# Optimization experiments

Measured on AMD Instinct MI355X. Metric: run time of the kernel, lower is better.

## Reference

```python
import jax, jax.numpy as jnp
import numpy as np

B, H = 1, 512
NVAR, NCLS = 16384, 65536
NP, NM = 4096, 4096
NEG = -1e30


def setup_inputs() -> dict:
    key = jax.random.key(0)
    ks = jax.random.split(key, 16)
    s = 0.02  # weight init scale
    return {
        "literal_emb": jax.random.normal(ks[0], (B, 2 * NVAR, H), jnp.float32),
        "clause_emb": jax.random.normal(ks[1], (B, NCLS, H), jnp.float32),
        "pos_idx": jax.random.randint(ks[2], (NP,), 0, NCLS),
        "neg_idx": jax.random.randint(ks[3], (NM,), 0, NCLS),
        "keep_mask": jax.random.randint(ks[4], (NP, NM), 0, 2).astype(bool),
        "taken_mask": jax.random.uniform(ks[5], (NP, NM)) < 0.01,  # sparse exclusion set
        "var_K_w": s * jax.random.normal(ks[6], (H, H), jnp.float32),
        "var_K_b": jnp.zeros((H,), jnp.float32),
        "var_Q_w": s * jax.random.normal(ks[7], (H, H), jnp.float32),
        "var_Q_b": jnp.zeros((H,), jnp.float32),
        "var_attn_w": s * jax.random.normal(ks[8], (1, H), jnp.float32),
        "var_attn_b": jnp.zeros((1,), jnp.float32),
        "W_Q_w": s * jax.random.normal(ks[9], (H, H), jnp.float32),
        "W_Q_b": jnp.zeros((H,), jnp.float32),
        "W_K_w": s * jax.random.normal(ks[10], (H, H), jnp.float32),
        "W_K_b": jnp.zeros((H,), jnp.float32),
    }


def reference(literal_emb, clause_emb, pos_idx, neg_idx, keep_mask, taken_mask,
              var_K_w, var_K_b, var_Q_w, var_Q_b, var_attn_w, var_attn_b,
              W_Q_w, W_Q_b, W_K_w, W_K_b):
    n_vars = literal_emb.shape[1] // 2
    # --- select_var: additive attention over positive literals ---
    K = literal_emb[:, :n_vars]                       # [B, V, H]
    K_t = K @ var_K_w.T + var_K_b                     # [B, V, H]
    Q = clause_emb.sum(axis=1)                        # [B, H] (C_aggr='sum')
    Q_t = Q @ var_Q_w.T + var_Q_b                     # [B, H]
    u = (jnp.tanh(K_t + Q_t[:, None, :]) @ var_attn_w.T + var_attn_b)[..., 0]  # [B, V]
    log_score = jax.nn.log_softmax(u, axis=-1)
    var_logp = jnp.max(log_score, axis=-1)            # [B]
    var_idx = jnp.argmax(log_score, axis=-1)          # [B]
    # --- clause-pair attention over pivot pos/neg clause pools ---
    q = clause_emb[:, pos_idx] @ W_Q_w.T + W_Q_b      # [B, NP, H]
    k = clause_emb[:, neg_idx] @ W_K_w.T + W_K_b      # [B, NM, H]
    h = q.shape[-1]
    scores = jnp.einsum('bnh,bmh->bnm', q, k) / jnp.sqrt(jnp.float32(h))
    # mask_grid_asym: drop invalid (keep_mask==0) and already-taken pairs, log-normalize
    valid = keep_mask & (~taken_mask)                 # [NP, NM]
    masked = jnp.where(valid[None], scores, jnp.float32(NEG))
    flat = masked.reshape(masked.shape[0], -1)        # [B, NP*NM]
    logp = jax.nn.log_softmax(flat, axis=-1)
    C_logp = jnp.max(logp, axis=-1)                   # [B]
    C_flat = jnp.argmax(logp, axis=-1)                # [B]
    M = scores.shape[-1]
    ci, cj = C_flat // M, C_flat % M
    c_idx_pos = pos_idx[ci]                           # map back to global clause ids
    c_idx_neg = neg_idx[cj]
    c_logp = C_logp + var_logp                        # [B]
    return (c_logp, c_idx_pos, c_idx_neg, var_idx)
```

## Files before the change

kernel.cpp:

```cpp
#include <hip/hip_runtime.h>
#include <hip/hip_bf16.h>
#include <math.h>

#define HH 512
#define NVARS 16384
#define NPOS 4096
#define NMS 4096
#define NEGV -1.0e30f
#define RSQRT_H 0.04419417382415922f

typedef unsigned short u16;
typedef unsigned char u8;
typedef __attribute__((ext_vector_type(8))) short bf16x8;
typedef __attribute__((ext_vector_type(4))) float f32x4;

struct SPart { float m; float s; int a; int pad; };

__device__ inline u16 f2bf(float f) {
  unsigned u = __float_as_uint(f);
  unsigned r = (u + 0x7fffu + ((u >> 16) & 1u)) >> 16;
  return (u16)r;
}
__device__ inline float bf2f(u16 h) { return __uint_as_float(((unsigned)h) << 16); }

__device__ inline void wreduce_maxidx(float& v, int& idx) {
#pragma unroll
  for (int m = 1; m < 64; m <<= 1) {
    float ov = __shfl_xor(v, m, 64);
    int oi = __shfl_xor(idx, m, 64);
    if (ov > v || (ov == v && oi < idx)) { v = ov; idx = oi; }
  }
}

__device__ inline float wreduce_sum(float v) {
#pragma unroll
  for (int m = 1; m < 64; m <<= 1) v += __shfl_xor(v, m, 64);
  return v;
}

__device__ __forceinline__ void stage_frag(const u16* src, u16* dst) {
  __builtin_amdgcn_global_load_lds(
      (const __attribute__((address_space(1))) void*)src,
      (__attribute__((address_space(3))) void*)dst, 16, 0, 0);
}

__device__ __forceinline__ void do_tofrag(
    const float* __restrict__ src, u16* __restrict__ hi, u16* __restrict__ lo,
    int frag, int lane) {
  const int R = frag >> 4, K = frag & 15;
  const float* p = src + (size_t)(R * 16 + (lane & 15)) * HH + K * 32 + (lane >> 4) * 8;
  float v[8];
  *(float4*)&v[0] = *(const float4*)p;
  *(float4*)&v[4] = *(const float4*)(p + 4);
  u16 h[8], l[8];
#pragma unroll
  for (int e = 0; e < 8; ++e) { h[e] = f2bf(v[e]); l[e] = f2bf(v[e] - bf2f(h[e])); }
  size_t base = (size_t)frag * 512 + (size_t)lane * 8;
  *(ushort4*)(hi + base) = *(ushort4*)&h[0];
  *(ushort4*)(hi + base + 4) = *(ushort4*)&h[4];
  *(ushort4*)(lo + base) = *(ushort4*)&l[0];
  *(ushort4*)(lo + base + 4) = *(ushort4*)&l[4];
}

#define MFMA16(A, B)                                                                 \
  _Pragma("unroll") for (int i_ = 0; i_ < 4; ++i_)                                   \
  _Pragma("unroll") for (int j_ = 0; j_ < 4; ++j_)                                   \
    acc[i_][j_] = __builtin_amdgcn_mfma_f32_16x16x32_bf16(A[i_], B[j_], acc[i_][j_], 0, 0, 0);

#define MFMAS(AH, AL, BH, BL)                                                        \
  do { MFMA16(AH, BH) MFMA16(AH, BL) MFMA16(AL, BH) } while (0)

#define LOADF(s, AH, AL, BH, BL, PAH, PAL, PBH, PBL)                                 \
  do {                                                                               \
    _Pragma("unroll") for (int f_ = 0; f_ < 4; ++f_) {                               \
      size_t oa_ = abase + (size_t)f_ * 8192 + (size_t)(s) * 512;                    \
      size_t ob_ = bbase + (size_t)f_ * 8192 + (size_t)(s) * 512;                    \
      AH[f_] = *(const bf16x8*)(PAH + oa_);                                          \
      AL[f_] = *(const bf16x8*)(PAL + oa_);                                          \
      BH[f_] = *(const bf16x8*)(PBH + ob_);                                          \
      BL[f_] = *(const bf16x8*)(PBL + ob_);                                          \
    }                                                                                \
  } while (0)

__global__ __launch_bounds__(256) void wtofrag_kernel(
    const float* __restrict__ varKw, u16* __restrict__ wkhi, u16* __restrict__ wklo,
    const float* __restrict__ WQw, u16* __restrict__ pwqhi, u16* __restrict__ pwqlo,
    const float* __restrict__ WKw, u16* __restrict__ pwkhi, u16* __restrict__ pwklo) {
  const int wb = blockIdx.x;
  const int m = wb >> 7;
  const int frag = (wb & 127) * 4 + (threadIdx.x >> 6);
  const float* src = (m == 0) ? varKw : (m == 1) ? WQw : WKw;
  u16* hi = (m == 0) ? wkhi : (m == 1) ? pwqhi : pwkhi;
  u16* lo = (m == 0) ? wklo : (m == 1) ? pwqlo : pwklo;
  do_tofrag(src, hi, lo, frag, threadIdx.x & 63);
}

__global__ __launch_bounds__(256, 3) void proj_kernel(
    const float* __restrict__ clause,
    const int* __restrict__ pos_idx, const int* __restrict__ neg_idx,
    const u16* __restrict__ pwqhi, const u16* __restrict__ pwqlo,
    const u16* __restrict__ pwkhi, const u16* __restrict__ pwklo,
    const float* __restrict__ bQ, const float* __restrict__ bK,
    u16* __restrict__ qhi, u16* __restrict__ qlo,
    u16* __restrict__ khi, u16* __restrict__ klo) {
  const int* __restrict__ idx = blockIdx.z ? neg_idx : pos_idx;
  const u16* __restrict__ whp = blockIdx.z ? pwkhi : pwqhi;
  const u16* __restrict__ wlp = blockIdx.z ? pwklo : pwqlo;
  const float* __restrict__ bias = blockIdx.z ? bK : bQ;
  u16* __restrict__ ohi = blockIdx.z ? khi : qhi;
  u16* __restrict__ olo = blockIdx.z ? klo : qlo;

  const int t = threadIdx.x, lane = t & 63, wid = t >> 6;
  const int wn = wid & 1, wm = wid >> 1;
  const int row0 = blockIdx.x * 128;
  const int col0 = blockIdx.y * 128;

  const float* bptr[4];
#pragma unroll
  for (int j = 0; j < 4; ++j) {
    int g = idx[row0 + wn * 64 + j * 16 + (lane & 15)];
    bptr[j] = clause + (size_t)g * HH + (lane >> 4) * 8;
  }
  const size_t abase = (size_t)((col0 >> 4) + wm * 4) * 8192 + (size_t)lane * 8;

  f32x4 acc[4][4] = {};
#pragma unroll
  for (int s = 0; s < 16; ++s) {
    float rB[4][8];
    bf16x8 aH[4], aL[4], bH[4], bL[4];
#pragma unroll
    for (int f = 0; f < 4; ++f) {
      *(float4*)&rB[f][0] = *(const float4*)(bptr[f] + s * 32);
      *(float4*)&rB[f][4] = *(const float4*)(bptr[f] + s * 32 + 4);
      size_t oa = abase + (size_t)f * 8192 + (size_t)s * 512;
      aH[f] = *(const bf16x8*)(whp + oa);
      aL[f] = *(const bf16x8*)(wlp + oa);
    }
#pragma unroll
    for (int f = 0; f < 4; ++f)
#pragma unroll
      for (int e = 0; e < 8; ++e) {
        float v = rB[f][e];
        u16 h = f2bf(v);
        bH[f][e] = (short)h;
        bL[f][e] = (short)f2bf(v - bf2f(h));
      }
    MFMA16(aH, bH)
    MFMA16(aL, bH)
    MFMA16(aH, bL)
  }

  const int q4 = lane >> 4;
#pragma unroll
  for (int i = 0; i < 4; ++i) {
    const int hbase = col0 + wm * 64 + i * 16 + q4 * 4;
    float b0 = bias[hbase + 0], b1 = bias[hbase + 1];
    float b2 = bias[hbase + 2], b3 = bias[hbase + 3];
    const int lane16 = (lane & 15) + ((i & 1) * 2 + (q4 >> 1)) * 16;
    const int sub = (q4 & 1) * 4;
#pragma unroll
    for (int j = 0; j < 4; ++j) {
      const int frag = ((row0 + wn * 64 + j * 16) >> 4) * 16 +
                       ((col0 + wm * 64 + i * 16) >> 5);
      size_t base = (size_t)frag * 512 + (size_t)lane16 * 8 + sub;
      ushort4 hv, lv;
      float v;
      v = acc[i][j][0] + b0; hv.x = f2bf(v); lv.x = f2bf(v - bf2f(hv.x));
      v = acc[i][j][1] + b1; hv.y = f2bf(v); lv.y = f2bf(v - bf2f(hv.y));
      v = acc[i][j][2] + b2; hv.z = f2bf(v); lv.z = f2bf(v - bf2f(hv.z));
      v = acc[i][j][3] + b3; hv.w = f2bf(v); lv.w = f2bf(v - bf2f(hv.w));
      *(ushort4*)(ohi + base) = hv;
      *(ushort4*)(olo + base) = lv;
    }
  }
}

__global__ __launch_bounds__(256, 3) void mega_kernel(
    const u16* __restrict__ qhi, const u16* __restrict__ qlo,
    const u16* __restrict__ khi, const u16* __restrict__ klo,
    const void* __restrict__ keep, const void* __restrict__ taken,
    SPart* __restrict__ parts,
    const float* __restrict__ clause, double* __restrict__ qpart,
    const float* __restrict__ lit, u16* __restrict__ lithi, u16* __restrict__ litlo) {
  __shared__ unsigned long long mrow[128][2];
  __shared__ float s_rv[4]; __shared__ int s_ri[4]; __shared__ float s_rs[4];
  __shared__ float s_bm; __shared__ int s_ba;

  const int id = blockIdx.x;
  const int t = threadIdx.x;
  const int lane = t & 63;
  const int wid = t >> 6;

  if (id >= 3072) {
    const int frag = (id - 3072) * 4 + wid;
    do_tofrag(lit, lithi, litlo, frag, lane);
    return;
  }
  if (id >= 1024) {
    const int qb = id - 1024;
    const int fg = t & 127;
    const int rh = t >> 7;
    const float* base = clause + ((size_t)qb * 32 + rh * 16) * HH + fg * 4;
    float4 v[16];
#pragma unroll
    for (int u = 0; u < 16; ++u)
      v[u] = *(const float4*)(base + (size_t)u * HH);
    double a0 = 0.0, a1 = 0.0, a2 = 0.0, a3 = 0.0;
#pragma unroll
    for (int u = 0; u < 16; ++u) {
      a0 += (double)v[u].x; a1 += (double)v[u].y;
      a2 += (double)v[u].z; a3 += (double)v[u].w;
    }
    double* o = qpart + (size_t)(qb * 2 + rh) * HH + fg * 4;
    o[0] = a0; o[1] = a1; o[2] = a2; o[3] = a3;
    return;
  }

  const int wn = wid & 1, wm = wid >> 1;

  const int bid = id;
  const int xcd = bid & 7, p = bid >> 3;
  const int sp = p >> 6, q = p & 63;
  const int g = xcd * 2 + sp;
  const int bx = (g & 3) * 8 + (q & 7);
  const int by = (g >> 2) * 8 + (q >> 3);

  const int n0 = by * 128;
  const int m0 = bx * 128;

  {
    const int r = t >> 1, half = t & 1;
    const unsigned* kw = (const unsigned*)keep;
    int f = 1;
#pragma unroll
    for (int i = 0; i < 16; ++i) f &= (kw[i] <= 1u);
    unsigned long long w = 0;
    if (!f) {
      const u8* kp = (const u8*)keep + (size_t)(n0 + r) * NMS + m0 + half * 64;
      const u8* tp = (const u8*)taken + (size_t)(n0 + r) * NMS + m0 + half * 64;
#pragma unroll
      for (int c = 0; c < 4; ++c) {
        uint4 kv = *(const uint4*)(kp + c * 16);
        uint4 tv = *(const uint4*)(tp + c * 16);
        unsigned kws[4] = {kv.x, kv.y, kv.z, kv.w};
        unsigned tws[4] = {tv.x, tv.y, tv.z, tv.w};
#pragma unroll
        for (int wi = 0; wi < 4; ++wi)
#pragma unroll
          for (int y = 0; y < 4; ++y) {
            unsigned kb = (kws[wi] >> (8 * y)) & 0xffu;
            unsigned tb = (tws[wi] >> (8 * y)) & 0xffu;
            w |= (unsigned long long)(kb && !tb) << (c * 16 + wi * 4 + y);
          }
      }
    } else {
      const unsigned* kp = (const unsigned*)keep + (size_t)(n0 + r) * NMS + m0 + half * 64;
      const unsigned* tp = (const unsigned*)taken + (size_t)(n0 + r) * NMS + m0 + half * 64;
#pragma unroll
      for (int c = 0; c < 16; ++c) {
        uint4 kv = *(const uint4*)(kp + c * 4);
        uint4 tv = *(const uint4*)(tp + c * 4);
        w |= (unsigned long long)(kv.x && !tv.x) << (c * 4 + 0);
        w |= (unsigned long long)(kv.y && !tv.y) << (c * 4 + 1);
        w |= (unsigned long long)(kv.z && !tv.z) << (c * 4 + 2);
        w |= (unsigned long long)(kv.w && !tv.w) << (c * 4 + 3);
      }
    }
    mrow[r][half] = w;
  }

  const size_t abase = (size_t)((n0 >> 4) + wn * 4) * 8192 + (size_t)lane * 8;
  const size_t bbase = (size_t)((m0 >> 4) + wm * 4) * 8192 + (size_t)lane * 8;

  f32x4 acc[4][4] = {};
#pragma unroll
  for (int s = 0; s < 16; ++s) {
    bf16x8 aH[4], aL[4], bH[4], bL[4];
    LOADF(s, aH, aL, bH, bL, qhi, qlo, khi, klo);
    MFMAS(aH, aL, bH, bL);
  }
  __syncthreads();

  const int rbase = wn * 64 + (lane >> 4) * 4;
  const int cb15 = (lane & 15);

  float mv = NEGV; int mi = 0x7fffffff;
#pragma unroll
  for (int i = 0; i < 4; ++i) {
#pragma unroll
    for (int r = 0; r < 4; ++r) {
      int rl = rbase + i * 16 + r;
      unsigned long long ww = mrow[rl][wm];
      int gb = (n0 + rl) * NMS + m0;
#pragma unroll
      for (int j = 0; j < 4; ++j) {
        int bit = j * 16 + cb15;
        int cl = wm * 64 + bit;
        float sv = acc[i][j][r] * RSQRT_H;
        acc[i][j][r] = sv;
        bool valid = ((ww >> bit) & 1ull) != 0;
        if (valid && (sv > mv || (sv == mv && gb + cl < mi))) { mv = sv; mi = gb + cl; }
      }
    }
  }
  wreduce_maxidx(mv, mi);
  if ((t & 63) == 0) { s_rv[wid] = mv; s_ri[wid] = mi; }
  __syncthreads();
  if (t == 0) {
    float bm = s_rv[0]; int ba = s_ri[0];
    for (int w = 1; w < 4; ++w)
      if (s_rv[w] > bm || (s_rv[w] == bm && s_ri[w] < ba)) { bm = s_rv[w]; ba = s_ri[w]; }
    s_bm = bm; s_ba = ba;
  }
  __syncthreads();
  const float bm = s_bm;

  float se = 0.f;
#pragma unroll
  for (int i = 0; i < 4; ++i) {
#pragma unroll
    for (int r = 0; r < 4; ++r) {
      int rl = rbase + i * 16 + r;
      unsigned long long ww = mrow[rl][wm];
#pragma unroll
      for (int j = 0; j < 4; ++j) {
        int bit = j * 16 + cb15;
        bool valid = ((ww >> bit) & 1ull) != 0;
        if (valid) se += __expf(acc[i][j][r] - bm);
      }
    }
  }
  se = wreduce_sum(se);
  if ((t & 63) == 0) s_rs[wid] = se;
  __syncthreads();
  if (t == 0) {
    SPart pt;
    pt.m = s_bm;
    pt.s = s_rs[0] + s_rs[1] + s_rs[2] + s_rs[3];
    pt.a = s_ba; pt.pad = 0;
    parts[by * 32 + bx] = pt;
  }
}

__global__ __launch_bounds__(256) void qred_kernel(
    const double* __restrict__ qpart, double* __restrict__ Qd) {
  __shared__ double red[256];
  const int t = threadIdx.x;
  const int h = blockIdx.x * 16 + (t & 15);
  const int chunk = t >> 4;
  double s = 0.0;
  for (int j0 = 0; j0 < 256; j0 += 8) {
    double v[8];
#pragma unroll
    for (int u = 0; u < 8; ++u)
      v[u] = qpart[(size_t)(chunk * 256 + j0 + u) * HH + h];
#pragma unroll
    for (int u = 0; u < 8; ++u) s += v[u];
  }
  red[t] = s;
  __syncthreads();
  for (int off = 8; off > 0; off >>= 1) {
    if (chunk < off) red[t] += red[t + off * 16];
    __syncthreads();
  }
  if (t < 16) Qd[blockIdx.x * 16 + t] = red[t];
}

__global__ __launch_bounds__(256) void prepmv_kernel(
    const double* __restrict__ Qd, const float* __restrict__ varQw,
    const float* __restrict__ varQb, const float* __restrict__ varKb,
    float* __restrict__ tvec) {
  __shared__ double red[256];
  const int t = threadIdx.x;
  const int h = blockIdx.x * 16 + (t & 15);
  const int chunk = t >> 4;
  const float* wrow = varQw + (size_t)h * HH + chunk * 32;
  const double* qd = Qd + chunk * 32;
  double s = 0.0;
  for (int j = 0; j < 32; ++j) s += qd[j] * (double)wrow[j];
  red[t] = s;
  __syncthreads();
  for (int off = 8; off > 0; off >>= 1) {
    if (chunk < off) red[t] += red[t + off * 16];
    __syncthreads();
  }
  if (t < 16) {
    int hh = blockIdx.x * 16 + t;
    tvec[hh] = (float)(red[t] + (double)varQb[hh] + (double)varKb[hh]);
  }
}

__global__ __launch_bounds__(256, 2) void ktu_kernel(
    const u16* __restrict__ lithi, const u16* __restrict__ litlo,
    const u16* __restrict__ wkhi, const u16* __restrict__ wklo,
    const float* __restrict__ tvec, const float* __restrict__ attnw,
    float* __restrict__ upart) {
  __shared__ __align__(16) u16 lds[2][4][8][512];
  const int t = threadIdx.x, lane = t & 63, wid = t >> 6;
  const int wn = wid & 1, wm = wid >> 1;
  const int row0 = blockIdx.x * 128;
  const int l8 = lane * 8;

  const u16* sa = (wid == 0) ? lithi : (wid == 1) ? litlo : (wid == 2) ? wkhi : wklo;
  const int rb = (wid < 2) ? (row0 >> 4) : (blockIdx.y * 8);
  const u16* sab = sa + (size_t)rb * 8192 + l8;

#define KSTAGE(buf, s)                                                        \
  _Pragma("unroll") for (int f_ = 0; f_ < 8; ++f_)                            \
    stage_frag(sab + (size_t)f_ * 8192 + (size_t)(s) * 512,                   \
               &lds[buf][wid][f_][0]);

  KSTAGE(0, 0)
  f32x4 acc[4][4] = {};
#pragma unroll
  for (int s = 0; s < 16; ++s) {
    __syncthreads();
    if (s < 15) { KSTAGE((s + 1) & 1, s + 1) }
    const int b = s & 1;
    bf16x8 aH[4], aL[4], bH[4], bL[4];
#pragma unroll
    for (int f = 0; f < 4; ++f) {
      aH[f] = *(const bf16x8*)&lds[b][0][wn * 4 + f][l8];
      aL[f] = *(const bf16x8*)&lds[b][1][wn * 4 + f][l8];
      bH[f] = *(const bf16x8*)&lds[b][2][wm * 4 + f][l8];
      bL[f] = *(const bf16x8*)&lds[b][3][wm * 4 + f][l8];
    }
    MFMAS(aH, aL, bH, bL);
  }
#undef KSTAGE

  const int cbase = blockIdx.y * 128 + wm * 64;
  float tv[4], aw[4];
#pragma unroll
  for (int j = 0; j < 4; ++j) {
    int c = cbase + j * 16 + (lane & 15);
    tv[j] = tvec[c]; aw[j] = attnw[c];
  }
  float us[4][4];
#pragma unroll
  for (int i = 0; i < 4; ++i)
#pragma unroll
    for (int r = 0; r < 4; ++r) {
      float s = 0.f;
#pragma unroll
      for (int j = 0; j < 4; ++j) {
        float x = acc[i][j][r] + tv[j];
        float th = 1.0f - 2.0f / (__expf(2.0f * x) + 1.0f);
        s += th * aw[j];
      }
      us[i][r] = s;
    }
#pragma unroll
  for (int m = 1; m < 16; m <<= 1)
#pragma unroll
    for (int i = 0; i < 4; ++i)
#pragma unroll
      for (int r = 0; r < 4; ++r) us[i][r] += __shfl_xor(us[i][r], m, 64);
  if ((lane & 15) == 0) {
#pragma unroll
    for (int i = 0; i < 4; ++i)
#pragma unroll
      for (int r = 0; r < 4; ++r) {
        int row = row0 + wn * 64 + i * 16 + (lane >> 4) * 4 + r;
        upart[(size_t)(blockIdx.y * 2 + wm) * NVARS + row] = us[i][r];
      }
  }
}

__global__ __launch_bounds__(256) void usum_kernel(
    const float* __restrict__ upart, SPart* __restrict__ uparts2) {
  __shared__ float s_rv[4]; __shared__ int s_ri[4]; __shared__ float s_rs[4];
  __shared__ float s_bm; __shared__ int s_ba;
  const int t = threadIdx.x;
  const int i = blockIdx.x * 256 + t;
  float u = 0.f;
#pragma unroll
  for (int p = 0; p < 8; ++p) u += upart[(size_t)p * NVARS + i];
  float mv = u; int mi = i;
  wreduce_maxidx(mv, mi);
  if ((t & 63) == 0) { s_rv[t >> 6] = mv; s_ri[t >> 6] = mi; }
  __syncthreads();
  if (t == 0) {
    float bm = s_rv[0]; int ba = s_ri[0];
    for (int w = 1; w < 4; ++w)
      if (s_rv[w] > bm || (s_rv[w] == bm && s_ri[w] < ba)) { bm = s_rv[w]; ba = s_ri[w]; }
    s_bm = bm; s_ba = ba;
  }
  __syncthreads();
  float se = __expf(u - s_bm);
  se = wreduce_sum(se);
  if ((t & 63) == 0) s_rs[t >> 6] = se;
  __syncthreads();
  if (t == 0) {
    SPart p;
    p.m = s_bm;
    p.s = s_rs[0] + s_rs[1] + s_rs[2] + s_rs[3];
    p.a = s_ba; p.pad = 0;
    uparts2[blockIdx.x] = p;
  }
}

__global__ __launch_bounds__(256) void final_kernel(
    const SPart* __restrict__ uparts2, const SPart* __restrict__ parts,
    const int* __restrict__ pos_idx, const int* __restrict__ neg_idx,
    float* __restrict__ out) {
  __shared__ float s_rv[4]; __shared__ int s_ri[4]; __shared__ float s_rs[4];
  __shared__ float s_umax; __shared__ int s_uarg; __shared__ float s_usum;
  __shared__ float s_gm; __shared__ int s_ga;
  const int t = threadIdx.x;

  float mv = -3.0e38f; int mi = 0x7fffffff;
  SPart up;
  if (t < 64) {
    up = uparts2[t];
    mv = up.m; mi = up.a;
  }
  wreduce_maxidx(mv, mi);
  if ((t & 63) == 0) { s_rv[t >> 6] = mv; s_ri[t >> 6] = mi; }
  __syncthreads();
  if (t == 0) {
    float bm = s_rv[0]; int ba = s_ri[0];
    for (int w = 1; w < 4; ++w)
      if (s_rv[w] > bm || (s_rv[w] == bm && s_ri[w] < ba)) { bm = s_rv[w]; ba = s_ri[w]; }
    s_umax = bm; s_uarg = ba;
  }
  __syncthreads();
  float se = (t < 64) ? up.s * __expf(up.m - s_umax) : 0.f;
  se = wreduce_sum(se);
  if ((t & 63) == 0) s_rs[t >> 6] = se;
  __syncthreads();
  if (t == 0) s_usum = s_rs[0] + s_rs[1] + s_rs[2] + s_rs[3];
  __syncthreads();

  mv = NEGV; mi = 0x7fffffff;
  for (int i = t; i < 1024; i += 256) {
    SPart p = parts[i];
    if (p.m > mv || (p.m == mv && p.a < mi)) { mv = p.m; mi = p.a; }
  }
  wreduce_maxidx(mv, mi);
  if ((t & 63) == 0) { s_rv[t >> 6] = mv; s_ri[t >> 6] = mi; }
  __syncthreads();
  if (t == 0) {
    float bm = s_rv[0]; int ba = s_ri[0];
    for (int w = 1; w < 4; ++w)
      if (s_rv[w] > bm || (s_rv[w] == bm && s_ri[w] < ba)) { bm = s_rv[w]; ba = s_ri[w]; }
    s_gm = bm; s_ga = ba;
  }
  __syncthreads();
  const float gm = s_gm;
  float ss = 0.f;
  for (int i = t; i < 1024; i += 256) {
    SPart p = parts[i];
    ss += p.s * __expf(p.m - gm);
  }
  ss = wreduce_sum(ss);
  if ((t & 63) == 0) s_rs[t >> 6] = ss;
  __syncthreads();
  if (t == 0) {
    float gsum = s_rs[0] + s_rs[1] + s_rs[2] + s_rs[3];
    float c_logp = -logf(gsum) - logf(s_usum);
    int ga = s_ga;
    if (ga == 0x7fffffff) ga = 0;
    int ci = ga >> 12, cj = ga & 4095;
    out[0] = c_logp;
    out[1] = (float)pos_idx[ci];
    out[2] = (float)neg_idx[cj];
    out[3] = (float)s_uarg;
  }
}

extern "C" void kernel_launch(void* const* d_in, const int* in_sizes, int n_in,
                              void* d_out, int out_size, void* d_ws, size_t ws_size,
                              hipStream_t stream) {
  (void)in_sizes; (void)n_in; (void)out_size; (void)ws_size;
  const float* lit    = (const float*)d_in[0];
  const float* clause = (const float*)d_in[1];
  const int* pos_idx  = (const int*)d_in[2];
  const int* neg_idx  = (const int*)d_in[3];
  const void* keep    = d_in[4];
  const void* taken   = d_in[5];
  const float* varKw  = (const float*)d_in[6];
  const float* varKb  = (const float*)d_in[7];
  const float* varQw  = (const float*)d_in[8];
  const float* varQb  = (const float*)d_in[9];
  const float* attnw  = (const float*)d_in[10];
  const float* WQw    = (const float*)d_in[12];
  const float* WQb    = (const float*)d_in[13];
  const float* WKw    = (const float*)d_in[14];
  const float* WKb    = (const float*)d_in[15];

  char* ws = (char*)d_ws;
  size_t off = 0;
  auto alloc = [&](size_t b) {
    char* p = ws + off;
    off = (off + b + 255) & ~(size_t)255;
    return p;
  };
  double* qpart              = (double*)alloc((size_t)4096 * HH * 8);
  double* Qd                 = (double*)alloc(HH * 8);
  float* tvec                = (float*)alloc(HH * 4);
  float* upart               = (float*)alloc(8 * (size_t)NVARS * 4);
  u16* qhi                   = (u16*)alloc((size_t)NPOS * HH * 2);
  u16* qlo                   = (u16*)alloc((size_t)NPOS * HH * 2);
  u16* khi                   = (u16*)alloc((size_t)NMS * HH * 2);
  u16* klo                   = (u16*)alloc((size_t)NMS * HH * 2);
  u16* wkhi                  = (u16*)alloc((size_t)HH * HH * 2);
  u16* wklo                  = (u16*)alloc((size_t)HH * HH * 2);
  u16* pwqhi                 = (u16*)alloc((size_t)HH * HH * 2);
  u16* pwqlo                 = (u16*)alloc((size_t)HH * HH * 2);
  u16* pwkhi                 = (u16*)alloc((size_t)HH * HH * 2);
  u16* pwklo                 = (u16*)alloc((size_t)HH * HH * 2);
  u16* lithi                 = (u16*)alloc((size_t)NVARS * HH * 2);
  u16* litlo                 = (u16*)alloc((size_t)NVARS * HH * 2);
  SPart* parts               = (SPart*)alloc(1024 * sizeof(SPart));
  SPart* uparts2             = (SPart*)alloc(64 * sizeof(SPart));

  wtofrag_kernel<<<384, 256, 0, stream>>>(varKw, wkhi, wklo,
                                          WQw, pwqhi, pwqlo,
                                          WKw, pwkhi, pwklo);
  proj_kernel<<<dim3(32, 4, 2), 256, 0, stream>>>(clause, pos_idx, neg_idx,
                                                  pwqhi, pwqlo, pwkhi, pwklo,
                                                  WQb, WKb,
                                                  qhi, qlo, khi, klo);
  mega_kernel<<<7168, 256, 0, stream>>>(qhi, qlo, khi, klo, keep, taken, parts,
                                        clause, qpart, lit, lithi, litlo);
  qred_kernel<<<32, 256, 0, stream>>>(qpart, Qd);
  prepmv_kernel<<<32, 256, 0, stream>>>(Qd, varQw, varQb, varKb, tvec);
  ktu_kernel<<<dim3(128, 4), 256, 0, stream>>>(lithi, litlo, wkhi, wklo,
                                               tvec, attnw, upart);
  usum_kernel<<<64, 256, 0, stream>>>(upart, uparts2);
  final_kernel<<<1, 256, 0, stream>>>(uparts2, parts, pos_idx, neg_idx,
                                      (float*)d_out);
}
```

Baseline: 258.2 us.

## Regroup kernels: fuse projection with prep work, scores with var attention

The q/k projection now runs in the same launch as the clause-sum and literal-to-fragment conversion (megaA). The clause-pair score GEMM with masked max/sum-exp now shares a launch with the literal key GEMM and tanh attention (megaB). The score GEMM also switches from direct global fragment loads to LDS double-buffered staging. This cuts launches and lets independent work fill the GPU together, at the cost of more LDS per block in megaB, which may lower occupancy.

Result: faster. 214.0 us (-17.1%).

```diff
diff --git a/kernel.cpp b/kernel.cpp
--- a/kernel.cpp
+++ b/kernel.cpp
@@ -69,18 +69,6 @@
 
 #define MFMAS(AH, AL, BH, BL)                                                        \
   do { MFMA16(AH, BH) MFMA16(AH, BL) MFMA16(AL, BH) } while (0)
-
-#define LOADF(s, AH, AL, BH, BL, PAH, PAL, PBH, PBL)                                 \
-  do {                                                                               \
-    _Pragma("unroll") for (int f_ = 0; f_ < 4; ++f_) {                               \
-      size_t oa_ = abase + (size_t)f_ * 8192 + (size_t)(s) * 512;                    \
-      size_t ob_ = bbase + (size_t)f_ * 8192 + (size_t)(s) * 512;                    \
-      AH[f_] = *(const bf16x8*)(PAH + oa_);                                          \
-      AL[f_] = *(const bf16x8*)(PAL + oa_);                                          \
-      BH[f_] = *(const bf16x8*)(PBH + ob_);                                          \
-      BL[f_] = *(const bf16x8*)(PBL + ob_);                                          \
-    }                                                                                \
-  } while (0)
 
 __global__ __launch_bounds__(256) void wtofrag_kernel(
     const float* __restrict__ varKw, u16* __restrict__ wkhi, u16* __restrict__ wklo,
@@ -95,25 +83,57 @@
   do_tofrag(src, hi, lo, frag, threadIdx.x & 63);
 }
 
-__global__ __launch_bounds__(256, 3) void proj_kernel(
+__global__ __launch_bounds__(256, 3) void megaA_kernel(
     const float* __restrict__ clause,
     const int* __restrict__ pos_idx, const int* __restrict__ neg_idx,
     const u16* __restrict__ pwqhi, const u16* __restrict__ pwqlo,
     const u16* __restrict__ pwkhi, const u16* __restrict__ pwklo,
     const float* __restrict__ bQ, const float* __restrict__ bK,
     u16* __restrict__ qhi, u16* __restrict__ qlo,
-    u16* __restrict__ khi, u16* __restrict__ klo) {
-  const int* __restrict__ idx = blockIdx.z ? neg_idx : pos_idx;
-  const u16* __restrict__ whp = blockIdx.z ? pwkhi : pwqhi;
-  const u16* __restrict__ wlp = blockIdx.z ? pwklo : pwqlo;
-  const float* __restrict__ bias = blockIdx.z ? bK : bQ;
-  u16* __restrict__ ohi = blockIdx.z ? khi : qhi;
-  u16* __restrict__ olo = blockIdx.z ? klo : qlo;
-
-  const int t = threadIdx.x, lane = t & 63, wid = t >> 6;
+    u16* __restrict__ khi, u16* __restrict__ klo,
+    double* __restrict__ qpart,
+    const float* __restrict__ lit, u16* __restrict__ lithi, u16* __restrict__ litlo) {
+  const int id = blockIdx.x;
+  const int t = threadIdx.x;
+  const int lane = t & 63, wid = t >> 6;
+
+  if (id >= 2304) {
+    const int frag = (id - 2304) * 4 + wid;
+    do_tofrag(lit, lithi, litlo, frag, lane);
+    return;
+  }
+  if (id >= 256) {
+    const int qb = id - 256;
+    const int fg = t & 127;
+    const int rh = t >> 7;
+    const float* base = clause + ((size_t)qb * 32 + rh * 16) * HH + fg * 4;
+    float4 v[16];
+#pragma unroll
+    for (int u = 0; u < 16; ++u)
+      v[u] = *(const float4*)(base + (size_t)u * HH);
+    double a0 = 0.0, a1 = 0.0, a2 = 0.0, a3 = 0.0;
+#pragma unroll
+    for (int u = 0; u < 16; ++u) {
+      a0 += (double)v[u].x; a1 += (double)v[u].y;
+      a2 += (double)v[u].z; a3 += (double)v[u].w;
+    }
+    double* o = qpart + (size_t)(qb * 2 + rh) * HH + fg * 4;
+    o[0] = a0; o[1] = a1; o[2] = a2; o[3] = a3;
+    return;
+  }
+
+  const int pid = id;
+  const int rowt = pid & 31, colt = (pid >> 5) & 3, z = pid >> 7;
+  const int* __restrict__ idx = z ? neg_idx : pos_idx;
+  const u16* __restrict__ whp = z ? pwkhi : pwqhi;
+  const u16* __restrict__ wlp = z ? pwklo : pwqlo;
+  const float* __restrict__ bias = z ? bK : bQ;
+  u16* __restrict__ ohi = z ? khi : qhi;
+  u16* __restrict__ olo = z ? klo : qlo;
+
   const int wn = wid & 1, wm = wid >> 1;
-  const int row0 = blockIdx.x * 128;
-  const int col0 = blockIdx.y * 128;
+  const int row0 = rowt * 128;
+  const int col0 = colt * 128;
 
   const float* bptr[4];
 #pragma unroll
@@ -172,173 +192,6 @@
       *(ushort4*)(ohi + base) = hv;
       *(ushort4*)(olo + base) = lv;
     }
-  }
-}
-
-__global__ __launch_bounds__(256, 3) void mega_kernel(
-    const u16* __restrict__ qhi, const u16* __restrict__ qlo,
-    const u16* __restrict__ khi, const u16* __restrict__ klo,
-    const void* __restrict__ keep, const void* __restrict__ taken,
-    SPart* __restrict__ parts,
-    const float* __restrict__ clause, double* __restrict__ qpart,
-    const float* __restrict__ lit, u16* __restrict__ lithi, u16* __restrict__ litlo) {
-  __shared__ unsigned long long mrow[128][2];
-  __shared__ float s_rv[4]; __shared__ int s_ri[4]; __shared__ float s_rs[4];
-  __shared__ float s_bm; __shared__ int s_ba;
-
-  const int id = blockIdx.x;
-  const int t = threadIdx.x;
-  const int lane = t & 63;
-  const int wid = t >> 6;
-
-  if (id >= 3072) {
-    const int frag = (id - 3072) * 4 + wid;
-    do_tofrag(lit, lithi, litlo, frag, lane);
-    return;
-  }
-  if (id >= 1024) {
-    const int qb = id - 1024;
-    const int fg = t & 127;
-    const int rh = t >> 7;
-    const float* base = clause + ((size_t)qb * 32 + rh * 16) * HH + fg * 4;
-    float4 v[16];
-#pragma unroll
-    for (int u = 0; u < 16; ++u)
-      v[u] = *(const float4*)(base + (size_t)u * HH);
-    double a0 = 0.0, a1 = 0.0, a2 = 0.0, a3 = 0.0;
-#pragma unroll
-    for (int u = 0; u < 16; ++u) {
-      a0 += (double)v[u].x; a1 += (double)v[u].y;
-      a2 += (double)v[u].z; a3 += (double)v[u].w;
-    }
-    double* o = qpart + (size_t)(qb * 2 + rh) * HH + fg * 4;
-    o[0] = a0; o[1] = a1; o[2] = a2; o[3] = a3;
-    return;
-  }
-
-  const int wn = wid & 1, wm = wid >> 1;
-
-  const int bid = id;
-  const int xcd = bid & 7, p = bid >> 3;
-  const int sp = p >> 6, q = p & 63;
-  const int g = xcd * 2 + sp;
-  const int bx = (g & 3) * 8 + (q & 7);
-  const int by = (g >> 2) * 8 + (q >> 3);
-
-  const int n0 = by * 128;
-  const int m0 = bx * 128;
-
-  {
-    const int r = t >> 1, half = t & 1;
-    const unsigned* kw = (const unsigned*)keep;
-    int f = 1;
-#pragma unroll
-    for (int i = 0; i < 16; ++i) f &= (kw[i] <= 1u);
-    unsigned long long w = 0;
-    if (!f) {
-      const u8* kp = (const u8*)keep + (size_t)(n0 + r) * NMS + m0 + half * 64;
-      const u8* tp = (const u8*)taken + (size_t)(n0 + r) * NMS + m0 + half * 64;
-#pragma unroll
-      for (int c = 0; c < 4; ++c) {
-        uint4 kv = *(const uint4*)(kp + c * 16);
-        uint4 tv = *(const uint4*)(tp + c * 16);
-        unsigned kws[4] = {kv.x, kv.y, kv.z, kv.w};
-        unsigned tws[4] = {tv.x, tv.y, tv.z, tv.w};
-#pragma unroll
-        for (int wi = 0; wi < 4; ++wi)
-#pragma unroll
-          for (int y = 0; y < 4; ++y) {
-            unsigned kb = (kws[wi] >> (8 * y)) & 0xffu;
-            unsigned tb = (tws[wi] >> (8 * y)) & 0xffu;
-            w |= (unsigned long long)(kb && !tb) << (c * 16 + wi * 4 + y);
-          }
-      }
-    } else {
-      const unsigned* kp = (const unsigned*)keep + (size_t)(n0 + r) * NMS + m0 + half * 64;
-      const unsigned* tp = (const unsigned*)taken + (size_t)(n0 + r) * NMS + m0 + half * 64;
-#pragma unroll
-      for (int c = 0; c < 16; ++c) {
-        uint4 kv = *(const uint4*)(kp + c * 4);
-        uint4 tv = *(const uint4*)(tp + c * 4);
-        w |= (unsigned long long)(kv.x && !tv.x) << (c * 4 + 0);
-        w |= (unsigned long long)(kv.y && !tv.y) << (c * 4 + 1);
-        w |= (unsigned long long)(kv.z && !tv.z) << (c * 4 + 2);
-        w |= (unsigned long long)(kv.w && !tv.w) << (c * 4 + 3);
-      }
-    }
-    mrow[r][half] = w;
-  }
-
-  const size_t abase = (size_t)((n0 >> 4) + wn * 4) * 8192 + (size_t)lane * 8;
-  const size_t bbase = (size_t)((m0 >> 4) + wm * 4) * 8192 + (size_t)lane * 8;
-
-  f32x4 acc[4][4] = {};
-#pragma unroll
-  for (int s = 0; s < 16; ++s) {
-    bf16x8 aH[4], aL[4], bH[4], bL[4];
-    LOADF(s, aH, aL, bH, bL, qhi, qlo, khi, klo);
-    MFMAS(aH, aL, bH, bL);
-  }
-  __syncthreads();
-
-  const int rbase = wn * 64 + (lane >> 4) * 4;
-  const int cb15 = (lane & 15);
-
-  float mv = NEGV; int mi = 0x7fffffff;
-#pragma unroll
-  for (int i = 0; i < 4; ++i) {
-#pragma unroll
-    for (int r = 0; r < 4; ++r) {
-      int rl = rbase + i * 16 + r;
-      unsigned long long ww = mrow[rl][wm];
-      int gb = (n0 + rl) * NMS + m0;
-#pragma unroll
-      for (int j = 0; j < 4; ++j) {
-        int bit = j * 16 + cb15;
-        int cl = wm * 64 + bit;
-        float sv = acc[i][j][r] * RSQRT_H;
-        acc[i][j][r] = sv;
-        bool valid = ((ww >> bit) & 1ull) != 0;
-        if (valid && (sv > mv || (sv == mv && gb + cl < mi))) { mv = sv; mi = gb + cl; }
-      }
-    }
-  }
-  wreduce_maxidx(mv, mi);
-  if ((t & 63) == 0) { s_rv[wid] = mv; s_ri[wid] = mi; }
-  __syncthreads();
-  if (t == 0) {
-    float bm = s_rv[0]; int ba = s_ri[0];
-    for (int w = 1; w < 4; ++w)
-      if (s_rv[w] > bm || (s_rv[w] == bm && s_ri[w] < ba)) { bm = s_rv[w]; ba = s_ri[w]; }
-    s_bm = bm; s_ba = ba;
-  }
-  __syncthreads();
-  const float bm = s_bm;
-
-  float se = 0.f;
-#pragma unroll
-  for (int i = 0; i < 4; ++i) {
-#pragma unroll
-    for (int r = 0; r < 4; ++r) {
-      int rl = rbase + i * 16 + r;
-      unsigned long long ww = mrow[rl][wm];
-#pragma unroll
-      for (int j = 0; j < 4; ++j) {
-        int bit = j * 16 + cb15;
-        bool valid = ((ww >> bit) & 1ull) != 0;
-        if (valid) se += __expf(acc[i][j][r] - bm);
-      }
-    }
-  }
-  se = wreduce_sum(se);
-  if ((t & 63) == 0) s_rs[wid] = se;
-  __syncthreads();
-  if (t == 0) {
-    SPart pt;
-    pt.m = s_bm;
-    pt.s = s_rs[0] + s_rs[1] + s_rs[2] + s_rs[3];
-    pt.a = s_ba; pt.pad = 0;
-    parts[by * 32 + bx] = pt;
   }
 }
 
@@ -390,32 +243,165 @@
   }
 }
 
-__global__ __launch_bounds__(256, 2) void ktu_kernel(
+__global__ __launch_bounds__(256, 2) void megaB_kernel(
+    const u16* __restrict__ qhi, const u16* __restrict__ qlo,
+    const u16* __restrict__ khi, const u16* __restrict__ klo,
+    const void* __restrict__ keep, const void* __restrict__ taken,
+    SPart* __restrict__ parts,
     const u16* __restrict__ lithi, const u16* __restrict__ litlo,
     const u16* __restrict__ wkhi, const u16* __restrict__ wklo,
     const float* __restrict__ tvec, const float* __restrict__ attnw,
     float* __restrict__ upart) {
   __shared__ __align__(16) u16 lds[2][4][8][512];
-  const int t = threadIdx.x, lane = t & 63, wid = t >> 6;
+  __shared__ unsigned long long mrow[128][2];
+  __shared__ float s_rv[4]; __shared__ int s_ri[4]; __shared__ float s_rs[4];
+  __shared__ float s_bm; __shared__ int s_ba;
+
+  const int id = blockIdx.x;
+  const int t = threadIdx.x;
+  const int lane = t & 63;
+  const int wid = t >> 6;
   const int wn = wid & 1, wm = wid >> 1;
-  const int row0 = blockIdx.x * 128;
   const int l8 = lane * 8;
 
-  const u16* sa = (wid == 0) ? lithi : (wid == 1) ? litlo : (wid == 2) ? wkhi : wklo;
-  const int rb = (wid < 2) ? (row0 >> 4) : (blockIdx.y * 8);
+  if (id >= 1024) {
+    const int kb = id - 1024;
+    const int rowt = kb >> 2, ht = kb & 3;
+    const int row0 = rowt * 128;
+
+    const u16* sa = (wid == 0) ? lithi : (wid == 1) ? litlo : (wid == 2) ? wkhi : wklo;
+    const int rb = (wid < 2) ? (row0 >> 4) : (ht * 8);
+    const u16* sab = sa + (size_t)rb * 8192 + l8;
+
+#define KSTAGE(buf, s)                                                        \
+    _Pragma("unroll") for (int f_ = 0; f_ < 8; ++f_)                          \
+      stage_frag(sab + (size_t)f_ * 8192 + (size_t)(s) * 512,                 \
+                 &lds[buf][wid][f_][0]);
+
+    KSTAGE(0, 0)
+    f32x4 acc[4][4] = {};
+#pragma unroll
+    for (int s = 0; s < 16; ++s) {
+      __syncthreads();
+      if (s < 15) { KSTAGE((s + 1) & 1, s + 1) }
+      const int b = s & 1;
+      bf16x8 aH[4], aL[4], bH[4], bL[4];
+#pragma unroll
+      for (int f = 0; f < 4; ++f) {
+        aH[f] = *(const bf16x8*)&lds[b][0][wn * 4 + f][l8];
+        aL[f] = *(const bf16x8*)&lds[b][1][wn * 4 + f][l8];
+        bH[f] = *(const bf16x8*)&lds[b][2][wm * 4 + f][l8];
+        bL[f] = *(const bf16x8*)&lds[b][3][wm * 4 + f][l8];
+      }
+      MFMAS(aH, aL, bH, bL);
+    }
+#undef KSTAGE
+
+    const int cbase = ht * 128 + wm * 64;
+    float tv[4], aw[4];
+#pragma unroll
+    for (int j = 0; j < 4; ++j) {
+      int c = cbase + j * 16 + (lane & 15);
+      tv[j] = tvec[c]; aw[j] = attnw[c];
+    }
+    float us[4][4];
+#pragma unroll
+    for (int i = 0; i < 4; ++i)
+#pragma unroll
+      for (int r = 0; r < 4; ++r) {
+        float s = 0.f;
+#pragma unroll
+        for (int j = 0; j < 4; ++j) {
+          float x = acc[i][j][r] + tv[j];
+          float th = 1.0f - 2.0f / (__expf(2.0f * x) + 1.0f);
+          s += th * aw[j];
+        }
+        us[i][r] = s;
+      }
+#pragma unroll
+    for (int m = 1; m < 16; m <<= 1)
+#pragma unroll
+      for (int i = 0; i < 4; ++i)
+#pragma unroll
+        for (int r = 0; r < 4; ++r) us[i][r] += __shfl_xor(us[i][r], m, 64);
+    if ((lane & 15) == 0) {
+#pragma unroll
+      for (int i = 0; i < 4; ++i)
+#pragma unroll
+        for (int r = 0; r < 4; ++r) {
+          int row = row0 + wn * 64 + i * 16 + (lane >> 4) * 4 + r;
+          upart[(size_t)(ht * 2 + wm) * NVARS + row] = us[i][r];
+        }
+    }
+    return;
+  }
+
+  const int bid = id;
+  const int xcd = bid & 7, p = bid >> 3;
+  const int sp = p >> 6, q = p & 63;
+  const int g = xcd * 2 + sp;
+  const int bx = (g & 3) * 8 + (q & 7);
+  const int by = (g >> 2) * 8 + (q >> 3);
+
+  const int n0 = by * 128;
+  const int m0 = bx * 128;
+
+  {
+    const int r = t >> 1, half = t & 1;
+    const unsigned* kw = (const unsigned*)keep;
+    int f = 1;
+#pragma unroll
+    for (int i = 0; i < 16; ++i) f &= (kw[i] <= 1u);
+    unsigned long long w = 0;
+    if (!f) {
+      const u8* kp = (const u8*)keep + (size_t)(n0 + r) * NMS + m0 + half * 64;
+      const u8* tp = (const u8*)taken + (size_t)(n0 + r) * NMS + m0 + half * 64;
+#pragma unroll
+      for (int c = 0; c < 4; ++c) {
+        uint4 kv = *(const uint4*)(kp + c * 16);
+        uint4 tv = *(const uint4*)(tp + c * 16);
+        unsigned kws[4] = {kv.x, kv.y, kv.z, kv.w};
+        unsigned tws[4] = {tv.x, tv.y, tv.z, tv.w};
+#pragma unroll
+        for (int wi = 0; wi < 4; ++wi)
+#pragma unroll
+          for (int y = 0; y < 4; ++y) {
+            unsigned kb = (kws[wi] >> (8 * y)) & 0xffu;
+            unsigned tb = (tws[wi] >> (8 * y)) & 0xffu;
+            w |= (unsigned long long)(kb && !tb) << (c * 16 + wi * 4 + y);
+          }
+      }
+    } else {
+      const unsigned* kp = (const unsigned*)keep + (size_t)(n0 + r) * NMS + m0 + half * 64;
+      const unsigned* tp = (const unsigned*)taken + (size_t)(n0 + r) * NMS + m0 + half * 64;
+#pragma unroll
+      for (int c = 0; c < 16; ++c) {
+        uint4 kv = *(const uint4*)(kp + c * 4);
+        uint4 tv = *(const uint4*)(tp + c * 4);
+        w |= (unsigned long long)(kv.x && !tv.x) << (c * 4 + 0);
+        w |= (unsigned long long)(kv.y && !tv.y) << (c * 4 + 1);
+        w |= (unsigned long long)(kv.z && !tv.z) << (c * 4 + 2);
+        w |= (unsigned long long)(kv.w && !tv.w) << (c * 4 + 3);
+      }
+    }
+    mrow[r][half] = w;
+  }
+
+  const u16* sa = (wid == 0) ? qhi : (wid == 1) ? qlo : (wid == 2) ? khi : klo;
+  const int rb = (wid < 2) ? (n0 >> 4) : (m0 >> 4);
   const u16* sab = sa + (size_t)rb * 8192 + l8;
 
-#define KSTAGE(buf, s)                                                        \
+#define SSTAGE(buf, s)                                                        \
   _Pragma("unroll") for (int f_ = 0; f_ < 8; ++f_)                            \
     stage_frag(sab + (size_t)f_ * 8192 + (size_t)(s) * 512,                   \
                &lds[buf][wid][f_][0]);
 
-  KSTAGE(0, 0)
+  SSTAGE(0, 0)
   f32x4 acc[4][4] = {};
 #pragma unroll
   for (int s = 0; s < 16; ++s) {
     __syncthreads();
-    if (s < 15) { KSTAGE((s + 1) & 1, s + 1) }
+    if (s < 15) { SSTAGE((s + 1) & 1, s + 1) }
     const int b = s & 1;
     bf16x8 aH[4], aL[4], bH[4], bL[4];
 #pragma unroll
@@ -427,43 +413,66 @@
     }
     MFMAS(aH, aL, bH, bL);
   }
-#undef KSTAGE
-
-  const int cbase = blockIdx.y * 128 + wm * 64;
-  float tv[4], aw[4];
-#pragma unroll
-  for (int j = 0; j < 4; ++j) {
-    int c = cbase + j * 16 + (lane & 15);
-    tv[j] = tvec[c]; aw[j] = attnw[c];
-  }
-  float us[4][4];
-#pragma unroll
-  for (int i = 0; i < 4; ++i)
+#undef SSTAGE
+
+  const int rbase = wn * 64 + (lane >> 4) * 4;
+  const int cb15 = (lane & 15);
+
+  float mv = NEGV; int mi = 0x7fffffff;
+#pragma unroll
+  for (int i = 0; i < 4; ++i) {
 #pragma unroll
     for (int r = 0; r < 4; ++r) {
-      float s = 0.f;
+      int rl = rbase + i * 16 + r;
+      unsigned long long ww = mrow[rl][wm];
+      int gb = (n0 + rl) * NMS + m0;
 #pragma unroll
       for (int j = 0; j < 4; ++j) {
-        float x = acc[i][j][r] + tv[j];
-        float th = 1.0f - 2.0f / (__expf(2.0f * x) + 1.0f);
-        s += th * aw[j];
+        int bit = j * 16 + cb15;
+        int cl = wm * 64 + bit;
+        float sv = acc[i][j][r] * RSQRT_H;
+        acc[i][j][r] = sv;
+        bool valid = ((ww >> bit) & 1ull) != 0;
+        if (valid && (sv > mv || (sv == mv && gb + cl < mi))) { mv = sv; mi = gb + cl; }
       }
-      us[i][r] = s;
-    }
-#pragma unroll
-  for (int m = 1; m < 16; m <<= 1)
-#pragma unroll
-    for (int i = 0; i < 4; ++i)
-#pragma unroll
-      for (int r = 0; r < 4; ++r) us[i][r] += __shfl_xor(us[i][r], m, 64);
-  if ((lane & 15) == 0) {
-#pragma unroll
-    for (int i = 0; i < 4; ++i)
-#pragma unroll
-      for (int r = 0; r < 4; ++r) {
-        int row = row0 + wn * 64 + i * 16 + (lane >> 4) * 4 + r;
-        upart[(size_t)(blockIdx.y * 2 + wm) * NVARS + row] = us[i][r];
+    }
+  }
+  wreduce_maxidx(mv, mi);
+  if ((t & 63) == 0) { s_rv[wid] = mv; s_ri[wid] = mi; }
+  __syncthreads();
+  if (t == 0) {
+    float bm = s_rv[0]; int ba = s_ri[0];
+    for (int w = 1; w < 4; ++w)
+      if (s_rv[w] > bm || (s_rv[w] == bm && s_ri[w] < ba)) { bm = s_rv[w]; ba = s_ri[w]; }
+    s_bm = bm; s_ba = ba;
+  }
+  __syncthreads();
+  const float bm = s_bm;
+
+  float se = 0.f;
+#pragma unroll
+  for (int i = 0; i < 4; ++i) {
+#pragma unroll
+    for (int r = 0; r < 4; ++r) {
+      int rl = rbase + i * 16 + r;
+      unsigned long long ww = mrow[rl][wm];
+#pragma unroll
+      for (int j = 0; j < 4; ++j) {
+        int bit = j * 16 + cb15;
+        bool valid = ((ww >> bit) & 1ull) != 0;
+        if (valid) se += __expf(acc[i][j][r] - bm);
       }
+    }
+  }
+  se = wreduce_sum(se);
+  if ((t & 63) == 0) s_rs[wid] = se;
+  __syncthreads();
+  if (t == 0) {
+    SPart pt;
+    pt.m = s_bm;
+    pt.s = s_rs[0] + s_rs[1] + s_rs[2] + s_rs[3];
+    pt.a = s_ba; pt.pad = 0;
+    parts[by * 32 + bx] = pt;
   }
 }
 
@@ -618,16 +627,15 @@
   wtofrag_kernel<<<384, 256, 0, stream>>>(varKw, wkhi, wklo,
                                           WQw, pwqhi, pwqlo,
                                           WKw, pwkhi, pwklo);
-  proj_kernel<<<dim3(32, 4, 2), 256, 0, stream>>>(clause, pos_idx, neg_idx,
-                                                  pwqhi, pwqlo, pwkhi, pwklo,
-                                                  WQb, WKb,
-                                                  qhi, qlo, khi, klo);
-  mega_kernel<<<7168, 256, 0, stream>>>(qhi, qlo, khi, klo, keep, taken, parts,
-                                        clause, qpart, lit, lithi, litlo);
+  megaA_kernel<<<6400, 256, 0, stream>>>(clause, pos_idx, neg_idx,
+                                         pwqhi, pwqlo, pwkhi, pwklo,
+                                         WQb, WKb, qhi, qlo, khi, klo,
+                                         qpart, lit, lithi, litlo);
   qred_kernel<<<32, 256, 0, stream>>>(qpart, Qd);
   prepmv_kernel<<<32, 256, 0, stream>>>(Qd, varQw, varQb, varKb, tvec);
-  ktu_kernel<<<dim3(128, 4), 256, 0, stream>>>(lithi, litlo, wkhi, wklo,
-                                               tvec, attnw, upart);
+  megaB_kernel<<<1536, 256, 0, stream>>>(qhi, qlo, khi, klo, keep, taken, parts,
+                                         lithi, litlo, wkhi, wklo,
+                                         tvec, attnw, upart);
   usum_kernel<<<64, 256, 0, stream>>>(upart, uparts2);
   final_kernel<<<1, 256, 0, stream>>>(uparts2, parts, pos_idx, neg_idx,
                                       (float*)d_out);
```
